# Kernel tuning notes

Measured on AMD Instinct MI355X. Metric: run time of the kernel, lower is better.

Reference implementation:

```python
import jax, jax.numpy as jnp
import numpy as np

C = 256       # planes
S = 4         # sub-spectral groups
N, F, T = 16, 64, 256
EPS = 1e-5
WQ = (8, 7)   # weight quant (bits, frac)
AQ = (8, 4)   # activation quant
AQ_SRAM = (8, 4)
BNMQ = (8, 7) # bn scale quant
BNBQ = (8, 4) # bn bias quant


def fixpoint(x, q):
    """Fixed-point quantize to q=(total_bits, frac_bits), straight-through estimator."""
    bits, frac = q
    scale = 2.0 ** frac
    qmax = 2.0 ** (bits - 1) - 1.0
    qmin = -(2.0 ** (bits - 1))
    qx = jnp.clip(jnp.round(x * scale), qmin, qmax) / scale
    return x + jax.lax.stop_gradient(qx - x)


def dwconv(x, w, pad):
    # x: [N,C,H,W], w: [C,1,kh,kw] depthwise (groups=C)
    return jax.lax.conv_general_dilated(
        x, w, window_strides=(1, 1), padding=pad,
        dimension_numbers=('NCHW', 'OIHW', 'NCHW'),
        feature_group_count=x.shape[1])


def qbn(x, gamma, beta, mean, var):
    # quantized inference batchnorm: y = x*m + b with m, b fixed-point
    m = fixpoint(gamma / jnp.sqrt(var + EPS), BNMQ)
    b = fixpoint(beta - mean * m, BNBQ)
    return x * m[None, :, None, None] + b[None, :, None, None]


def setup_inputs() -> dict:
    key = jax.random.key(0)
    ks = jax.random.split(key, 12)
    return {
        'x': jax.random.normal(ks[0], (N, C, F, T), dtype=jnp.float32),
        'w_freq': jax.random.normal(ks[1], (C, 1, 3, 1), dtype=jnp.float32) * 0.2,
        'ssn_gamma': 1.0 + 0.1 * jax.random.normal(ks[2], (C * S,), dtype=jnp.float32),
        'ssn_beta': 0.1 * jax.random.normal(ks[3], (C * S,), dtype=jnp.float32),
        'ssn_mean': 0.1 * jax.random.normal(ks[4], (C * S,), dtype=jnp.float32),
        'ssn_var': jax.random.uniform(ks[5], (C * S,), minval=0.5, maxval=1.5, dtype=jnp.float32),
        'w_temp': jax.random.normal(ks[6], (C, 1, 1, 3), dtype=jnp.float32) * 0.2,
        'bn2_gamma': 1.0 + 0.1 * jax.random.normal(ks[7], (C,), dtype=jnp.float32),
        'bn2_beta': 0.1 * jax.random.normal(ks[8], (C,), dtype=jnp.float32),
        'bn2_mean': 0.1 * jax.random.normal(ks[9], (C,), dtype=jnp.float32),
        'bn2_var': jax.random.uniform(ks[10], (C,), minval=0.5, maxval=1.5, dtype=jnp.float32),
        'w_1x1': jax.random.normal(ks[11], (C, C, 1, 1), dtype=jnp.float32) * 0.06,
    }


def reference(x, w_freq, ssn_gamma, ssn_beta, ssn_mean, ssn_var,
              w_temp, bn2_gamma, bn2_beta, bn2_mean, bn2_var, w_1x1):
    # freq depthwise conv (3,1), pad (1,0), quantized weights
    out = dwconv(x, fixpoint(w_freq, WQ), ((1, 1), (0, 0)))
    out = fixpoint(out, AQ)
    # sub-spectral norm: view [N, C*S, F//S, T], BN, view back
    n, c, f, t = out.shape
    out = out.reshape(n, c * S, f // S, t)
    out = qbn(out, ssn_gamma, ssn_beta, ssn_mean, ssn_var)
    out = out.reshape(n, c, f, t)
    out = fixpoint(out, AQ)
    auxilary = fixpoint(out, AQ_SRAM)
    # mean over freq, keepdim
    out = out.mean(axis=2, keepdims=True)
    out = fixpoint(out, AQ)
    # temporal depthwise conv (1,3), pad (0,1)
    out = dwconv(out, fixpoint(w_temp, WQ), ((0, 0), (1, 1)))
    out = fixpoint(out, AQ)
    out = qbn(out, bn2_gamma, bn2_beta, bn2_mean, bn2_var)
    out = fixpoint(out, AQ)
    out = jax.nn.relu(out)  # 'swish' in source is nn.ReLU()
    out = fixpoint(out, AQ)
    # 1x1 pointwise conv via einsum over channels
    out = jnp.einsum('nchw,oc->nohw', out, fixpoint(w_1x1, WQ)[:, :, 0, 0])
    out = fixpoint(out, AQ)
    out = auxilary + out  # broadcasts over freq dim
    out = fixpoint(out, AQ)
    return jax.nn.relu(out)
```

## Files before the change

kernel.cpp:

```cpp
#include <hip/hip_runtime.h>
#include <hip/hip_bf16.h>

#define N_ 16
#define C_ 256
#define F_ 64
#define T_ 256

__device__ __forceinline__ float quantq(float x, float scale, float inv_scale) {
    float v = rintf(x * scale);
    v = fminf(fmaxf(v, -128.0f), 127.0f);
    return v * inv_scale;
}

template<bool FINAL>
__global__ __launch_bounds__(256) void plane_kernel(
    const float* __restrict__ x,
    const float* __restrict__ wf,
    const float* __restrict__ ssn_g,
    const float* __restrict__ ssn_b,
    const float* __restrict__ ssn_mu,
    const float* __restrict__ ssn_va,
    signed char* __restrict__ mean_s8,
    const signed char* __restrict__ y_s8,
    float* __restrict__ out)
{
    const int plane = blockIdx.x;
    const int c = plane & (C_ - 1);
    const int t = threadIdx.x;

    const float* xp = x + (size_t)plane * (F_ * T_) + t;

    const float w0 = quantq(wf[c * 3 + 0], 128.f, 1.f / 128.f);
    const float w1 = quantq(wf[c * 3 + 1], 128.f, 1.f / 128.f);
    const float w2 = quantq(wf[c * 3 + 2], 128.f, 1.f / 128.f);

    float m[4], b[4];
    #pragma unroll
    for (int g = 0; g < 4; ++g) {
        const int cs = c * 4 + g;
        const float mm = quantq(ssn_g[cs] * rsqrtf(ssn_va[cs] + 1e-5f),
                                128.f, 1.f / 128.f);
        m[g] = mm;
        b[g] = quantq(ssn_b[cs] - ssn_mu[cs] * mm, 16.f, 1.f / 16.f);
    }

    float yv = 0.f;
    if (FINAL) yv = (float)y_s8[plane * T_ + t] * (1.f / 16.f);

    float xm = 0.f;
    float x0 = xp[0];
    float sum = 0.f;

    float* op = FINAL ? (out + (size_t)plane * (F_ * T_) + t) : nullptr;

    #pragma unroll 8
    for (int f = 0; f < F_; ++f) {
        const float xn = (f < F_ - 1) ? xp[(f + 1) * T_] : 0.f;
        float conv = xm * w0 + x0 * w1 + xn * w2;
        float q1 = quantq(conv, 16.f, 1.f / 16.f);
        const int g = f >> 4;
        float aux = quantq(q1 * m[g] + b[g], 16.f, 1.f / 16.f);
        if (FINAL) {
            float o = quantq(aux + yv, 16.f, 1.f / 16.f);
            o = fmaxf(o, 0.f);
            op[f * T_] = o;
        } else {
            sum += aux;
        }
        xm = x0; x0 = xn;
    }

    if (!FINAL) {
        const float mn = quantq(sum * (1.f / 64.f), 16.f, 1.f / 16.f);
        mean_s8[plane * T_ + t] = (signed char)(int)rintf(mn * 16.f);
    }
}

#define TT_ 16
__global__ __launch_bounds__(256) void mean_path_kernel(
    const signed char* __restrict__ mean_s8,
    const float* __restrict__ wt,
    const float* __restrict__ g2,
    const float* __restrict__ b2,
    const float* __restrict__ mu2,
    const float* __restrict__ va2,
    const float* __restrict__ w1,
    signed char* __restrict__ y_s8)
{
    const int n = blockIdx.x >> 4;
    const int tt = (blockIdx.x & 15) * TT_;
    const int tid = threadIdx.x;

    __shared__ float z[TT_][C_];

    {
        const int c = tid;
        const float wq0 = quantq(wt[c * 3 + 0], 128.f, 1.f / 128.f);
        const float wq1 = quantq(wt[c * 3 + 1], 128.f, 1.f / 128.f);
        const float wq2 = quantq(wt[c * 3 + 2], 128.f, 1.f / 128.f);
        const float m2 = quantq(g2[c] * rsqrtf(va2[c] + 1e-5f),
                                128.f, 1.f / 128.f);
        const float bb2 = quantq(b2[c] - mu2[c] * m2, 16.f, 1.f / 16.f);
        const signed char* mp = mean_s8 + (n * C_ + c) * T_;
        #pragma unroll
        for (int j = 0; j < TT_; ++j) {
            const int t = tt + j;
            const float a = (t > 0)       ? (float)mp[t - 1] * (1.f / 16.f) : 0.f;
            const float bmid =              (float)mp[t]     * (1.f / 16.f);
            const float d = (t < T_ - 1)  ? (float)mp[t + 1] * (1.f / 16.f) : 0.f;
            float tc = a * wq0 + bmid * wq1 + d * wq2;
            float v = quantq(tc, 16.f, 1.f / 16.f);
            v = quantq(v * m2 + bb2, 16.f, 1.f / 16.f);
            v = fmaxf(v, 0.f);
            z[j][c] = v;
        }
    }
    __syncthreads();
    {
        const int o = tid;
        float acc[TT_];
        #pragma unroll
        for (int j = 0; j < TT_; ++j) acc[j] = 0.f;
        const float* wrow = w1 + o * C_;
        for (int c = 0; c < C_; ++c) {
            const float wv = quantq(wrow[c], 128.f, 1.f / 128.f);
            #pragma unroll
            for (int j = 0; j < TT_; ++j) acc[j] += z[j][c] * wv;
        }
        signed char* yp = y_s8 + (n * C_ + o) * T_ + tt;
        #pragma unroll
        for (int j = 0; j < TT_; ++j) {
            const float q = quantq(acc[j], 16.f, 1.f / 16.f);
            yp[j] = (signed char)(int)rintf(q * 16.f);
        }
    }
}

extern "C" void kernel_launch(void* const* d_in, const int* in_sizes, int n_in,
                              void* d_out, int out_size, void* d_ws, size_t ws_size,
                              hipStream_t stream) {
    const float* x       = (const float*)d_in[0];
    const float* w_freq  = (const float*)d_in[1];
    const float* ssn_g   = (const float*)d_in[2];
    const float* ssn_b   = (const float*)d_in[3];
    const float* ssn_mu  = (const float*)d_in[4];
    const float* ssn_va  = (const float*)d_in[5];
    const float* w_temp  = (const float*)d_in[6];
    const float* g2      = (const float*)d_in[7];
    const float* b2      = (const float*)d_in[8];
    const float* mu2     = (const float*)d_in[9];
    const float* va2     = (const float*)d_in[10];
    const float* w_1x1   = (const float*)d_in[11];
    float* out = (float*)d_out;

    signed char* mean_s8 = (signed char*)d_ws;
    signed char* y_s8    = mean_s8 + (size_t)N_ * C_ * T_;

    dim3 blk(256);
    plane_kernel<false><<<dim3(N_ * C_), blk, 0, stream>>>(
        x, w_freq, ssn_g, ssn_b, ssn_mu, ssn_va, mean_s8, nullptr, nullptr);
    mean_path_kernel<<<dim3(N_ * (T_ / TT_)), blk, 0, stream>>>(
        mean_s8, w_temp, g2, b2, mu2, va2, w_1x1, y_s8);
    plane_kernel<true><<<dim3(N_ * C_), blk, 0, stream>>>(
        x, w_freq, ssn_g, ssn_b, ssn_mu, ssn_va, nullptr, y_s8, out);
}
```

Measured before the change: 543.6 us.

## Store int8 aux activations instead of recomputing conv pass; vectorize plane kernels

The first pass now writes the quantized sub-spectral-norm activations as int8 codes alongside the per-plane mean. The final pass becomes a lightweight combine that reads those int8 codes instead of re-reading the fp32 input and recomputing the conv and norm. Both plane kernels use one wave per plane with float4/char4 accesses. The cost is an extra int8 workspace buffer of the full activation size.

Measured after the change: 534.3 us. Within noise of the previous version (-1.7%).

```diff
diff --git a/kernel.cpp b/kernel.cpp
--- a/kernel.cpp
+++ b/kernel.cpp
@@ -1,79 +1,94 @@
 #include <hip/hip_runtime.h>
-#include <hip/hip_bf16.h>
 
 #define N_ 16
 #define C_ 256
 #define F_ 64
 #define T_ 256
 
-__device__ __forceinline__ float quantq(float x, float scale, float inv_scale) {
-    float v = rintf(x * scale);
-    v = fminf(fmaxf(v, -128.0f), 127.0f);
-    return v * inv_scale;
-}
-
-template<bool FINAL>
-__global__ __launch_bounds__(256) void plane_kernel(
+__device__ __forceinline__ float clampf(float v, float lo, float hi) {
+    return fminf(fmaxf(v, lo), hi);
+}
+
+__device__ __forceinline__ float qcode(float x, float scale) {
+    return clampf(rintf(x * scale), -128.f, 127.f);
+}
+
+__global__ __launch_bounds__(256) void aux_mean_kernel(
     const float* __restrict__ x,
     const float* __restrict__ wf,
     const float* __restrict__ ssn_g,
     const float* __restrict__ ssn_b,
     const float* __restrict__ ssn_mu,
     const float* __restrict__ ssn_va,
-    signed char* __restrict__ mean_s8,
-    const signed char* __restrict__ y_s8,
-    float* __restrict__ out)
+    signed char* __restrict__ aux_s8,
+    signed char* __restrict__ mean_s8)
 {
-    const int plane = blockIdx.x;
+    const int wave = threadIdx.x >> 6;
+    const int lane = threadIdx.x & 63;
+    const int plane = blockIdx.x * 4 + wave;
     const int c = plane & (C_ - 1);
-    const int t = threadIdx.x;
-
-    const float* xp = x + (size_t)plane * (F_ * T_) + t;
-
-    const float w0 = quantq(wf[c * 3 + 0], 128.f, 1.f / 128.f);
-    const float w1 = quantq(wf[c * 3 + 1], 128.f, 1.f / 128.f);
-    const float w2 = quantq(wf[c * 3 + 2], 128.f, 1.f / 128.f);
-
-    float m[4], b[4];
-    #pragma unroll
+    const int t0 = lane * 4;
+
+    const float4* xp = (const float4*)(x + (size_t)plane * (F_ * T_) + t0);
+    signed char*  ap = aux_s8 + (size_t)plane * (F_ * T_) + t0;
+
+    const float w0 = qcode(wf[c * 3 + 0], 128.f) * (1.f / 128.f);
+    const float w1 = qcode(wf[c * 3 + 1], 128.f) * (1.f / 128.f);
+    const float w2 = qcode(wf[c * 3 + 2], 128.f) * (1.f / 128.f);
+
+    float4 xm = {0.f, 0.f, 0.f, 0.f};
+    float4 x0 = xp[0];
+    int s0 = 0, s1 = 0, s2 = 0, s3 = 0;
+
+    int f = 0;
     for (int g = 0; g < 4; ++g) {
         const int cs = c * 4 + g;
-        const float mm = quantq(ssn_g[cs] * rsqrtf(ssn_va[cs] + 1e-5f),
-                                128.f, 1.f / 128.f);
-        m[g] = mm;
-        b[g] = quantq(ssn_b[cs] - ssn_mu[cs] * mm, 16.f, 1.f / 16.f);
-    }
-
-    float yv = 0.f;
-    if (FINAL) yv = (float)y_s8[plane * T_ + t] * (1.f / 16.f);
-
-    float xm = 0.f;
-    float x0 = xp[0];
-    float sum = 0.f;
-
-    float* op = FINAL ? (out + (size_t)plane * (F_ * T_) + t) : nullptr;
-
-    #pragma unroll 8
-    for (int f = 0; f < F_; ++f) {
-        const float xn = (f < F_ - 1) ? xp[(f + 1) * T_] : 0.f;
-        float conv = xm * w0 + x0 * w1 + xn * w2;
-        float q1 = quantq(conv, 16.f, 1.f / 16.f);
-        const int g = f >> 4;
-        float aux = quantq(q1 * m[g] + b[g], 16.f, 1.f / 16.f);
-        if (FINAL) {
-            float o = quantq(aux + yv, 16.f, 1.f / 16.f);
-            o = fmaxf(o, 0.f);
-            op[f * T_] = o;
-        } else {
-            sum += aux;
-        }
-        xm = x0; x0 = xn;
-    }
-
-    if (!FINAL) {
-        const float mn = quantq(sum * (1.f / 64.f), 16.f, 1.f / 16.f);
-        mean_s8[plane * T_ + t] = (signed char)(int)rintf(mn * 16.f);
-    }
+        const float m = qcode(ssn_g[cs] * rsqrtf(ssn_va[cs] + 1e-5f), 128.f) * (1.f / 128.f);
+        const float b = qcode(ssn_b[cs] - ssn_mu[cs] * m, 16.f) * (1.f / 16.f);
+        #pragma unroll 4
+        for (int fi = 0; fi < 16; ++fi, ++f) {
+            float4 xn;
+            if (f < F_ - 1) xn = xp[(f + 1) * (T_ / 4)];
+            else            xn = make_float4(0.f, 0.f, 0.f, 0.f);
+
+            float ka0, ka1, ka2, ka3;
+            {
+                float conv = xm.x * w0 + x0.x * w1 + xn.x * w2;
+                float q1 = qcode(conv, 16.f) * (1.f / 16.f);
+                ka0 = qcode(q1 * m + b, 16.f);
+            }
+            {
+                float conv = xm.y * w0 + x0.y * w1 + xn.y * w2;
+                float q1 = qcode(conv, 16.f) * (1.f / 16.f);
+                ka1 = qcode(q1 * m + b, 16.f);
+            }
+            {
+                float conv = xm.z * w0 + x0.z * w1 + xn.z * w2;
+                float q1 = qcode(conv, 16.f) * (1.f / 16.f);
+                ka2 = qcode(q1 * m + b, 16.f);
+            }
+            {
+                float conv = xm.w * w0 + x0.w * w1 + xn.w * w2;
+                float q1 = qcode(conv, 16.f) * (1.f / 16.f);
+                ka3 = qcode(q1 * m + b, 16.f);
+            }
+            const int i0 = (int)ka0, i1 = (int)ka1, i2 = (int)ka2, i3 = (int)ka3;
+            s0 += i0; s1 += i1; s2 += i2; s3 += i3;
+            char4 cv;
+            cv.x = (signed char)i0; cv.y = (signed char)i1;
+            cv.z = (signed char)i2; cv.w = (signed char)i3;
+            *(char4*)(ap + f * T_) = cv;
+
+            xm = x0; x0 = xn;
+        }
+    }
+
+    char4 mv;
+    mv.x = (signed char)(int)clampf(rintf((float)s0 * (1.f / 64.f)), -128.f, 127.f);
+    mv.y = (signed char)(int)clampf(rintf((float)s1 * (1.f / 64.f)), -128.f, 127.f);
+    mv.z = (signed char)(int)clampf(rintf((float)s2 * (1.f / 64.f)), -128.f, 127.f);
+    mv.w = (signed char)(int)clampf(rintf((float)s3 * (1.f / 64.f)), -128.f, 127.f);
+    *(char4*)(mean_s8 + (size_t)plane * T_ + t0) = mv;
 }
 
 #define TT_ 16
@@ -95,22 +110,21 @@
 
     {
         const int c = tid;
-        const float wq0 = quantq(wt[c * 3 + 0], 128.f, 1.f / 128.f);
-        const float wq1 = quantq(wt[c * 3 + 1], 128.f, 1.f / 128.f);
-        const float wq2 = quantq(wt[c * 3 + 2], 128.f, 1.f / 128.f);
-        const float m2 = quantq(g2[c] * rsqrtf(va2[c] + 1e-5f),
-                                128.f, 1.f / 128.f);
-        const float bb2 = quantq(b2[c] - mu2[c] * m2, 16.f, 1.f / 16.f);
+        const float wq0 = qcode(wt[c * 3 + 0], 128.f) * (1.f / 128.f);
+        const float wq1 = qcode(wt[c * 3 + 1], 128.f) * (1.f / 128.f);
+        const float wq2 = qcode(wt[c * 3 + 2], 128.f) * (1.f / 128.f);
+        const float m2 = qcode(g2[c] * rsqrtf(va2[c] + 1e-5f), 128.f) * (1.f / 128.f);
+        const float bb2 = qcode(b2[c] - mu2[c] * m2, 16.f) * (1.f / 16.f);
         const signed char* mp = mean_s8 + (n * C_ + c) * T_;
         #pragma unroll
         for (int j = 0; j < TT_; ++j) {
             const int t = tt + j;
-            const float a = (t > 0)       ? (float)mp[t - 1] * (1.f / 16.f) : 0.f;
-            const float bmid =              (float)mp[t]     * (1.f / 16.f);
-            const float d = (t < T_ - 1)  ? (float)mp[t + 1] * (1.f / 16.f) : 0.f;
+            const float a    = (t > 0)      ? (float)mp[t - 1] * (1.f / 16.f) : 0.f;
+            const float bmid =                (float)mp[t]     * (1.f / 16.f);
+            const float d    = (t < T_ - 1) ? (float)mp[t + 1] * (1.f / 16.f) : 0.f;
             float tc = a * wq0 + bmid * wq1 + d * wq2;
-            float v = quantq(tc, 16.f, 1.f / 16.f);
-            v = quantq(v * m2 + bb2, 16.f, 1.f / 16.f);
+            float v = qcode(tc, 16.f) * (1.f / 16.f);
+            v = qcode(v * m2 + bb2, 16.f) * (1.f / 16.f);
             v = fmaxf(v, 0.f);
             z[j][c] = v;
         }
@@ -123,16 +137,47 @@
         for (int j = 0; j < TT_; ++j) acc[j] = 0.f;
         const float* wrow = w1 + o * C_;
         for (int c = 0; c < C_; ++c) {
-            const float wv = quantq(wrow[c], 128.f, 1.f / 128.f);
+            const float wv = qcode(wrow[c], 128.f) * (1.f / 128.f);
             #pragma unroll
             for (int j = 0; j < TT_; ++j) acc[j] += z[j][c] * wv;
         }
         signed char* yp = y_s8 + (n * C_ + o) * T_ + tt;
         #pragma unroll
         for (int j = 0; j < TT_; ++j) {
-            const float q = quantq(acc[j], 16.f, 1.f / 16.f);
-            yp[j] = (signed char)(int)rintf(q * 16.f);
-        }
+            yp[j] = (signed char)(int)qcode(acc[j], 16.f);
+        }
+    }
+}
+
+__global__ __launch_bounds__(256) void combine_kernel(
+    const signed char* __restrict__ aux_s8,
+    const signed char* __restrict__ y_s8,
+    float* __restrict__ out)
+{
+    const int wave = threadIdx.x >> 6;
+    const int lane = threadIdx.x & 63;
+    const int plane = blockIdx.x * 4 + wave;
+    const int t0 = lane * 4;
+
+    const char4 yk = *(const char4*)(y_s8 + (size_t)plane * T_ + t0);
+    const int y0 = yk.x, y1 = yk.y, y2 = yk.z, y3 = yk.w;
+
+    const char4* ap = (const char4*)(aux_s8 + (size_t)plane * (F_ * T_) + t0);
+    float4* op = (float4*)(out + (size_t)plane * (F_ * T_) + t0);
+
+    #pragma unroll 8
+    for (int f = 0; f < F_; ++f) {
+        const char4 ak = ap[f * (T_ / 4)];
+        const int o0 = min(127, max(0, (int)ak.x + y0));
+        const int o1 = min(127, max(0, (int)ak.y + y1));
+        const int o2 = min(127, max(0, (int)ak.z + y2));
+        const int o3 = min(127, max(0, (int)ak.w + y3));
+        float4 ov;
+        ov.x = (float)o0 * (1.f / 16.f);
+        ov.y = (float)o1 * (1.f / 16.f);
+        ov.z = (float)o2 * (1.f / 16.f);
+        ov.w = (float)o3 * (1.f / 16.f);
+        op[f * (T_ / 4)] = ov;
     }
 }
 
@@ -153,14 +198,15 @@
     const float* w_1x1   = (const float*)d_in[11];
     float* out = (float*)d_out;
 
-    signed char* mean_s8 = (signed char*)d_ws;
+    signed char* aux_s8  = (signed char*)d_ws;
+    signed char* mean_s8 = aux_s8 + (size_t)N_ * C_ * F_ * T_;
     signed char* y_s8    = mean_s8 + (size_t)N_ * C_ * T_;
 
     dim3 blk(256);
-    plane_kernel<false><<<dim3(N_ * C_), blk, 0, stream>>>(
-        x, w_freq, ssn_g, ssn_b, ssn_mu, ssn_va, mean_s8, nullptr, nullptr);
+    aux_mean_kernel<<<dim3(N_ * C_ / 4), blk, 0, stream>>>(
+        x, w_freq, ssn_g, ssn_b, ssn_mu, ssn_va, aux_s8, mean_s8);
     mean_path_kernel<<<dim3(N_ * (T_ / TT_)), blk, 0, stream>>>(
         mean_s8, w_temp, g2, b2, mu2, va2, w_1x1, y_s8);
-    plane_kernel<true><<<dim3(N_ * C_), blk, 0, stream>>>(
-        x, w_freq, ssn_g, ssn_b, ssn_mu, ssn_va, nullptr, y_s8, out);
-}
+    combine_kernel<<<dim3(N_ * C_ / 4), blk, 0, stream>>>(
+        aux_s8, y_s8, out);
+}
```
